# Optimization experiments

Hardware: AMD Instinct MI355X
Metric: run time of the kernel (lower is better)

The kernel has to match this reference:

```python
import jax, jax.numpy as jnp
import numpy as np

B, S, H, KVH, D, MD = 4, 4096, 2, 1, 2, 5  # batch, seq, heads, kv heads, head_dim, model_dim
EPS, SCALE = 1e-6, 16.0


def _rmsnorm(t):
    # RMSNormNoWeight with scale=16.0 over last dim
    var = jnp.mean(t * t, axis=-1, keepdims=True)
    return SCALE * t * jax.lax.rsqrt(var + EPS)


def _rope(t, cos, sin):
    # t: (B, S, h, D); cos/sin: (S, D//2). Complex multiply on interleaved pairs.
    tr, ti = t[..., 0::2], t[..., 1::2]
    c = cos[None, :, None, :]
    s = sin[None, :, None, :]
    out_r = tr * c - ti * s
    out_i = tr * s + ti * c
    return jnp.stack([out_r, out_i], axis=-1).reshape(t.shape)


def setup_inputs() -> dict:
    key = jax.random.key(0)
    ks = jax.random.split(key, 9)
    return {
        "x": jax.random.normal(ks[0], (B, S, MD), jnp.float32),
        "freqs": jax.random.normal(ks[1], (S, D // 2), jnp.float32),
        "shared_qk_v": jax.random.normal(ks[2], (MD,), jnp.float32),
        "shared_v_v": jax.random.normal(ks[3], (MD,), jnp.float32),
        "shared_o_v": jax.random.normal(ks[4], (H * D,), jnp.float32),
        "shared_vproj_u": jax.random.normal(ks[5], (KVH * D,), jnp.float32),
        "q_u": jax.random.normal(ks[6], (H * D,), jnp.float32),
        "k_u": jax.random.normal(ks[7], (KVH * D,), jnp.float32),
        "o_u": jax.random.normal(ks[8], (MD,), jnp.float32),
    }


def reference(x, freqs, shared_qk_v, shared_v_v, shared_o_v, shared_vproj_u, q_u, k_u, o_u):
    b, s = x.shape[0], x.shape[1]
    # rank-1 projections: (x . v) outer u
    s_qk = jnp.sum(x * shared_qk_v, axis=-1, keepdims=True)  # (B,S,1) shared by q and k
    q = (s_qk * q_u).reshape(b, s, H, D)
    k = (s_qk * k_u).reshape(b, s, KVH, D)
    s_v = jnp.sum(x * shared_v_v, axis=-1, keepdims=True)
    v = (s_v * shared_vproj_u).reshape(b, s, KVH, D)
    # qk-norm + rotary
    q = _rmsnorm(q)
    k = _rmsnorm(k)
    cos, sin = jnp.cos(freqs), jnp.sin(freqs)
    q = _rope(q, cos, sin)
    k = _rope(k, cos, sin)
    # (B,h,S,D)
    q = q.transpose(0, 2, 1, 3)
    k = k.transpose(0, 2, 1, 3)
    v = v.transpose(0, 2, 1, 3)
    # GQA repeat kv heads
    k = jnp.repeat(k, H // KVH, axis=1)
    v = jnp.repeat(v, H // KVH, axis=1)
    scores = jnp.einsum('bhqd,bhkd->bhqk', q, k) / jnp.sqrt(jnp.float32(D))
    probs = jax.nn.softmax(scores, axis=-1)
    out = jnp.einsum('bhqk,bhkd->bhqd', probs, v)
    out = out.transpose(0, 2, 1, 3).reshape(b, s, H * D)
    # rank-1 output projection
    s_o = jnp.sum(out * shared_o_v, axis=-1, keepdims=True)
    return s_o * o_u  # (B,S,MODEL_DIM)
```

## Files before the change

kernel.cpp:

```cpp
#include <hip/hip_runtime.h>
#include <math.h>


#define BQ 4
#define SQ 4096
#define MDQ 5
#define EPSQ 1e-6f
#define SCALEQ 16.0f
#define L2E 1.4426950408889634f
#define ISQ2 0.70710678118654752f

typedef float v2f __attribute__((ext_vector_type(2)));

__device__ __forceinline__ float fast_exp2(float x) {
#if __has_builtin(__builtin_amdgcn_exp2f)
    return __builtin_amdgcn_exp2f(x);
#else
    return __expf(x * 0.6931471805599453f);
#endif
}

__global__ __launch_bounds__(256)
void ca_prep(const float* __restrict__ x, const float* __restrict__ freqs,
             const float* __restrict__ qk_v, const float* __restrict__ v_v,
             const float* __restrict__ k_u, float4* __restrict__ pqc)
{
    const int idx = blockIdx.x * 256 + threadIdx.x;
    const int j   = idx & (SQ - 1);

    const float w0 = k_u[0], w1 = k_u[1];
    const float mk = 0.5f * (w0 * w0 + w1 * w1);

    const float qk0 = qk_v[0], qk1 = qk_v[1], qk2 = qk_v[2], qk3 = qk_v[3], qk4 = qk_v[4];
    const float vv0 = v_v[0],  vv1 = v_v[1],  vv2 = v_v[2],  vv3 = v_v[3],  vv4 = v_v[4];

    const float* xr = x + (size_t)idx * MDQ;
    const float x0 = xr[0], x1 = xr[1], x2 = xr[2], x3 = xr[3], x4 = xr[4];
    const float a  = x0*qk0 + x1*qk1 + x2*qk2 + x3*qk3 + x4*qk4;
    const float sv = x0*vv0 + x1*vv1 + x2*vv2 + x3*vv3 + x4*vv4;

    float sj, cj;
    __sincosf(freqs[j], &sj, &cj);
    const float mu = SCALEQ * a * rsqrtf(a * a * mk + EPSQ);
    pqc[idx] = make_float4(mu * cj, mu * sj, sv, sv);
}

#define BLOCK 256
#define RSETS 4
#define RPT 2
#define ROWSB (RSETS * RPT)
#define TILES (SQ / ROWSB)
#define KTILE 256
#define NKT (SQ / KTILE)
#define JPT (KTILE / 64)

__global__ __launch_bounds__(BLOCK)
void ca_main(const float* __restrict__ x,
             const float* __restrict__ freqs,
             const float* __restrict__ qk_v,
             const float* __restrict__ o_v,
             const float* __restrict__ vproj_u,
             const float* __restrict__ q_u,
             const float* __restrict__ k_u,
             const float* __restrict__ o_u,
             const float4* __restrict__ pqc,
             float* __restrict__ out)
{
    __shared__ float4 sKey[2][KTILE];

    const int tid = threadIdx.x;
    const int sp  = tid & 63;
    const int rs  = tid >> 6;
    const int bx  = blockIdx.x;
    const int b   = bx / TILES;
    const int tile = bx % TILES;
    const int i0  = tile * ROWSB + rs * RPT;

    const float w0 = k_u[0], w1 = k_u[1];
    const float mk  = 0.5f * (w0 * w0 + w1 * w1);
    const float Mmu = SCALEQ * rsqrtf(mk);

    const float qk0 = qk_v[0], qk1 = qk_v[1], qk2 = qk_v[2], qk3 = qk_v[3], qk4 = qk_v[4];
    const float u00 = q_u[0], u01 = q_u[1], u10 = q_u[2], u11 = q_u[3];
    const float m0 = 0.5f * (u00 * u00 + u01 * u01);
    const float m1 = 0.5f * (u10 * u10 + u11 * u11);
    const float A0 = u00 * w0 + u01 * w1, B0 = u01 * w0 - u00 * w1;
    const float A1 = u10 * w0 + u11 * w1, B1 = u11 * w0 - u10 * w1;

    v2f al[RPT], be[RPT], Cc[RPT];
#pragma unroll
    for (int k = 0; k < RPT; ++k) {
        const int i = i0 + k;
        const float* xi = x + (size_t)(b * SQ + i) * MDQ;
        const float ai = xi[0]*qk0 + xi[1]*qk1 + xi[2]*qk2 + xi[3]*qk3 + xi[4]*qk4;
        float si, ci;
        __sincosf(freqs[i], &si, &ci);
        const float lam0 = SCALEQ * ai * rsqrtf(ai * ai * m0 + EPSQ);
        const float lam1 = SCALEQ * ai * rsqrtf(ai * ai * m1 + EPSQ);
        const float a0  = lam0 * (A0 * ci - B0 * si) * ISQ2;
        const float b0_ = lam0 * (A0 * si + B0 * ci) * ISQ2;
        const float a1  = lam1 * (A1 * ci - B1 * si) * ISQ2;
        const float b1_ = lam1 * (A1 * si + B1 * ci) * ISQ2;
        const float r0 = sqrtf(a0 * a0 + b0_ * b0_);
        const float r1 = sqrtf(a1 * a1 + b1_ * b1_);
        al[k] = (v2f){a0 * L2E, a1 * L2E};
        be[k] = (v2f){b0_ * L2E, b1_ * L2E};
        Cc[k] = (v2f){-r0 * Mmu * L2E, -r1 * Mmu * L2E};
    }

    const float4* __restrict__ gsrc = pqc + (size_t)b * SQ + tid;

    float4 stage = gsrc[0];
    sKey[0][tid] = stage;
    __syncthreads();

    v2f l[RPT], n[RPT];
#pragma unroll
    for (int k = 0; k < RPT; ++k) { l[k] = (v2f){0.f, 0.f}; n[k] = (v2f){0.f, 0.f}; }

    for (int t = 0; t < NKT; ++t) {
        const int cur = t & 1;
        if (t + 1 < NKT) stage = gsrc[(size_t)(t + 1) * KTILE];

        const float4* kb = &sKey[cur][sp];
#pragma unroll
        for (int jj = 0; jj < JPT; ++jj) {
            const float4 v = kb[jj * 64];
            const v2f vx = (v2f){v.x, v.x};
            const v2f vy = (v2f){v.y, v.y};
            const v2f vz = (v2f){v.z, v.w};
#pragma unroll
            for (int k = 0; k < RPT; ++k) {
                const v2f s = al[k] * vx + (be[k] * vy + Cc[k]);
                v2f e;
                e.x = fast_exp2(s.x);
                e.y = fast_exp2(s.y);
                l[k] += e;
                n[k] += e * vz;
            }
        }

        if (t + 1 < NKT) {
            sKey[cur ^ 1][tid] = stage;
            __syncthreads();
        }
    }

#pragma unroll
    for (int m = 1; m < 64; m <<= 1) {
#pragma unroll
        for (int k = 0; k < RPT; ++k) {
            l[k].x += __shfl_xor(l[k].x, m, 64);
            l[k].y += __shfl_xor(l[k].y, m, 64);
            n[k].x += __shfl_xor(n[k].x, m, 64);
            n[k].y += __shfl_xor(n[k].y, m, 64);
        }
    }

    if (sp < RPT) {
        const int k = sp;
        const float L0 = fmaxf(l[k].x, 1e-30f);
        const float L1 = fmaxf(l[k].y, 1e-30f);
        const float W0 = n[k].x / L0, W1 = n[k].y / L1;

        const float p0 = vproj_u[0], p1 = vproj_u[1];
        const float d0 = p0 * o_v[0] + p1 * o_v[1];
        const float d1 = p0 * o_v[2] + p1 * o_v[3];
        const float so = W0 * d0 + W1 * d1;

        float* orow = out + (size_t)(b * SQ + i0 + k) * MDQ;
        orow[0] = so * o_u[0];
        orow[1] = so * o_u[1];
        orow[2] = so * o_u[2];
        orow[3] = so * o_u[3];
        orow[4] = so * o_u[4];
    }
}

#define FROWS 32
#define FSPLIT 8
#define FJSUB (SQ / FSPLIT)
#define FTILES (SQ / FROWS)

__global__ __launch_bounds__(256)
void ca_fallback(const float* __restrict__ x,
                 const float* __restrict__ freqs,
                 const float* __restrict__ qk_v,
                 const float* __restrict__ v_v,
                 const float* __restrict__ o_v,
                 const float* __restrict__ vproj_u,
                 const float* __restrict__ q_u,
                 const float* __restrict__ k_u,
                 const float* __restrict__ o_u,
                 float* __restrict__ out)
{
    __shared__ float2 sPQ[SQ];
    __shared__ float  sCv[SQ];
    __shared__ float4 sRed[FROWS][FSPLIT];

    const int tid  = threadIdx.x;
    const int b    = blockIdx.x / FTILES;
    const int tile = blockIdx.x % FTILES;

    const float w0 = k_u[0], w1 = k_u[1];
    const float mk  = 0.5f * (w0 * w0 + w1 * w1);
    const float Mmu = SCALEQ * rsqrtf(mk);

    const float qk0 = qk_v[0], qk1 = qk_v[1], qk2 = qk_v[2], qk3 = qk_v[3], qk4 = qk_v[4];
    const float vv0 = v_v[0],  vv1 = v_v[1],  vv2 = v_v[2],  vv3 = v_v[3],  vv4 = v_v[4];

    for (int k = 0; k < SQ / 256; ++k) {
        const int j = tid + k * 256;
        const float* xr = x + (size_t)(b * SQ + j) * MDQ;
        const float x0 = xr[0], x1 = xr[1], x2 = xr[2], x3 = xr[3], x4 = xr[4];
        const float a  = x0*qk0 + x1*qk1 + x2*qk2 + x3*qk3 + x4*qk4;
        const float sv = x0*vv0 + x1*vv1 + x2*vv2 + x3*vv3 + x4*vv4;
        float sj, cj;
        __sincosf(freqs[j], &sj, &cj);
        const float mu = SCALEQ * a * rsqrtf(a * a * mk + EPSQ);
        sPQ[j] = make_float2(mu * cj, mu * sj);
        sCv[j] = sv;
    }

    const int row = tid & (FROWS - 1);
    const int sp  = tid / FROWS;
    const int i   = tile * FROWS + row;

    const float u00 = q_u[0], u01 = q_u[1], u10 = q_u[2], u11 = q_u[3];
    const float m0 = 0.5f * (u00 * u00 + u01 * u01);
    const float m1 = 0.5f * (u10 * u10 + u11 * u11);
    const float A0 = u00 * w0 + u01 * w1, B0 = u01 * w0 - u00 * w1;
    const float A1 = u10 * w0 + u11 * w1, B1 = u11 * w0 - u10 * w1;

    const float* xi = x + (size_t)(b * SQ + i) * MDQ;
    const float ai = xi[0]*qk0 + xi[1]*qk1 + xi[2]*qk2 + xi[3]*qk3 + xi[4]*qk4;
    float si, ci;
    __sincosf(freqs[i], &si, &ci);
    const float lam0 = SCALEQ * ai * rsqrtf(ai * ai * m0 + EPSQ);
    const float lam1 = SCALEQ * ai * rsqrtf(ai * ai * m1 + EPSQ);
    const float alr0 = lam0 * (A0 * ci - B0 * si) * ISQ2;
    const float ber0 = lam0 * (A0 * si + B0 * ci) * ISQ2;
    const float alr1 = lam1 * (A1 * ci - B1 * si) * ISQ2;
    const float ber1 = lam1 * (A1 * si + B1 * ci) * ISQ2;
    const float r0 = sqrtf(alr0 * alr0 + ber0 * ber0);
    const float r1 = sqrtf(alr1 * alr1 + ber1 * ber1);
    const float al0 = alr0 * L2E, be0 = ber0 * L2E, C0 = -r0 * Mmu * L2E;
    const float al1 = alr1 * L2E, be1 = ber1 * L2E, C1 = -r1 * Mmu * L2E;

    __syncthreads();

    const float2* __restrict__ pq  = sPQ + sp * FJSUB;
    const float*  __restrict__ cvp = sCv + sp * FJSUB;
    float l0 = 0.f, n0 = 0.f, l1 = 0.f, n1 = 0.f;
#pragma unroll 8
    for (int jj = 0; jj < FJSUB; ++jj) {
        const float2 v = pq[jj];
        const float cv = cvp[jj];
        const float s0 = fmaf(al0, v.x, fmaf(be0, v.y, C0));
        const float s1 = fmaf(al1, v.x, fmaf(be1, v.y, C1));
        const float e0 = fast_exp2(s0);
        const float e1 = fast_exp2(s1);
        l0 += e0; n0 = fmaf(e0, cv, n0);
        l1 += e1; n1 = fmaf(e1, cv, n1);
    }

    sRed[row][sp] = make_float4(l0, n0, l1, n1);
    __syncthreads();

    if (tid < FROWS) {
        float L0 = 0.f, N0 = 0.f, L1 = 0.f, N1 = 0.f;
#pragma unroll
        for (int s = 0; s < FSPLIT; ++s) {
            const float4 t = sRed[tid][s];
            L0 += t.x; N0 += t.y; L1 += t.z; N1 += t.w;
        }
        L0 = fmaxf(L0, 1e-30f);
        L1 = fmaxf(L1, 1e-30f);
        const float W0 = N0 / L0, W1 = N1 / L1;
        const float p0 = vproj_u[0], p1 = vproj_u[1];
        const float d0 = p0 * o_v[0] + p1 * o_v[1];
        const float d1 = p0 * o_v[2] + p1 * o_v[3];
        const float so = W0 * d0 + W1 * d1;

        const int ig = tile * FROWS + tid;
        float* orow = out + (size_t)(b * SQ + ig) * MDQ;
        orow[0] = so * o_u[0];
        orow[1] = so * o_u[1];
        orow[2] = so * o_u[2];
        orow[3] = so * o_u[3];
        orow[4] = so * o_u[4];
    }
}

extern "C" void kernel_launch(void* const* d_in, const int* in_sizes, int n_in,
                              void* d_out, int out_size, void* d_ws, size_t ws_size,
                              hipStream_t stream) {
    (void)in_sizes; (void)n_in; (void)out_size;
    const float* x       = (const float*)d_in[0];
    const float* freqs   = (const float*)d_in[1];
    const float* qk_v    = (const float*)d_in[2];
    const float* v_v     = (const float*)d_in[3];
    const float* o_v     = (const float*)d_in[4];
    const float* vproj_u = (const float*)d_in[5];
    const float* q_u     = (const float*)d_in[6];
    const float* k_u     = (const float*)d_in[7];
    const float* o_u     = (const float*)d_in[8];
    float* out = (float*)d_out;

    const size_t pqc_bytes = (size_t)BQ * SQ * sizeof(float4);
    if (ws_size >= pqc_bytes) {
        float4* pqc = (float4*)d_ws;
        hipLaunchKernelGGL(ca_prep, dim3(BQ * SQ / 256), dim3(256), 0, stream,
                           x, freqs, qk_v, v_v, k_u, pqc);
        hipLaunchKernelGGL(ca_main, dim3(BQ * TILES), dim3(BLOCK), 0, stream,
                           x, freqs, qk_v, o_v, vproj_u, q_u, k_u, o_u, pqc, out);
    } else {
        hipLaunchKernelGGL(ca_fallback, dim3(BQ * FTILES), dim3(256), 0, stream,
                           x, freqs, qk_v, v_v, o_v, vproj_u, q_u, k_u, o_u, out);
    }
}
```

Measured before the change: 94.46 us.

## Fuse key preprocessing into main attention kernel with full-sequence LDS

Merges the separate key-preparation kernel into the attention kernel. Each 1024-thread block computes all keys for its batch directly into a 64KB shared buffer and then scans them without per-tile double buffering or repeated barriers. This removes a launch, the workspace write and read, and the per-tile synchronisation. In exchange, every block recomputes the key preprocessing, and the large LDS footprint limits how many blocks fit per CU. The workspace fallback path is deleted.

```diff
diff --git a/kernel.cpp b/kernel.cpp
--- a/kernel.cpp
+++ b/kernel.cpp
@@ -20,72 +20,62 @@
 #endif
 }
 
-__global__ __launch_bounds__(256)
-void ca_prep(const float* __restrict__ x, const float* __restrict__ freqs,
-             const float* __restrict__ qk_v, const float* __restrict__ v_v,
-             const float* __restrict__ k_u, float4* __restrict__ pqc)
+#define BLOCK 1024
+#define WAVES 16
+#define RPT 2
+#define ROWSB (WAVES * RPT)
+#define TILES (SQ / ROWSB)
+#define KPT (SQ / BLOCK)
+#define JPT (SQ / 64)
+
+__global__ __launch_bounds__(BLOCK, 8)
+void ca_fused(const float* __restrict__ x,
+              const float* __restrict__ freqs,
+              const float* __restrict__ qk_v,
+              const float* __restrict__ v_v,
+              const float* __restrict__ o_v,
+              const float* __restrict__ vproj_u,
+              const float* __restrict__ q_u,
+              const float* __restrict__ k_u,
+              const float* __restrict__ o_u,
+              float* __restrict__ out)
 {
-    const int idx = blockIdx.x * 256 + threadIdx.x;
-    const int j   = idx & (SQ - 1);
-
-    const float w0 = k_u[0], w1 = k_u[1];
-    const float mk = 0.5f * (w0 * w0 + w1 * w1);
-
-    const float qk0 = qk_v[0], qk1 = qk_v[1], qk2 = qk_v[2], qk3 = qk_v[3], qk4 = qk_v[4];
-    const float vv0 = v_v[0],  vv1 = v_v[1],  vv2 = v_v[2],  vv3 = v_v[3],  vv4 = v_v[4];
-
-    const float* xr = x + (size_t)idx * MDQ;
-    const float x0 = xr[0], x1 = xr[1], x2 = xr[2], x3 = xr[3], x4 = xr[4];
-    const float a  = x0*qk0 + x1*qk1 + x2*qk2 + x3*qk3 + x4*qk4;
-    const float sv = x0*vv0 + x1*vv1 + x2*vv2 + x3*vv3 + x4*vv4;
-
-    float sj, cj;
-    __sincosf(freqs[j], &sj, &cj);
-    const float mu = SCALEQ * a * rsqrtf(a * a * mk + EPSQ);
-    pqc[idx] = make_float4(mu * cj, mu * sj, sv, sv);
-}
-
-#define BLOCK 256
-#define RSETS 4
-#define RPT 2
-#define ROWSB (RSETS * RPT)
-#define TILES (SQ / ROWSB)
-#define KTILE 256
-#define NKT (SQ / KTILE)
-#define JPT (KTILE / 64)
-
-__global__ __launch_bounds__(BLOCK)
-void ca_main(const float* __restrict__ x,
-             const float* __restrict__ freqs,
-             const float* __restrict__ qk_v,
-             const float* __restrict__ o_v,
-             const float* __restrict__ vproj_u,
-             const float* __restrict__ q_u,
-             const float* __restrict__ k_u,
-             const float* __restrict__ o_u,
-             const float4* __restrict__ pqc,
-             float* __restrict__ out)
-{
-    __shared__ float4 sKey[2][KTILE];
+    __shared__ float4 sKey[SQ];
 
     const int tid = threadIdx.x;
     const int sp  = tid & 63;
-    const int rs  = tid >> 6;
+    const int w   = tid >> 6;
     const int bx  = blockIdx.x;
     const int b   = bx / TILES;
     const int tile = bx % TILES;
-    const int i0  = tile * ROWSB + rs * RPT;
 
     const float w0 = k_u[0], w1 = k_u[1];
     const float mk  = 0.5f * (w0 * w0 + w1 * w1);
     const float Mmu = SCALEQ * rsqrtf(mk);
 
     const float qk0 = qk_v[0], qk1 = qk_v[1], qk2 = qk_v[2], qk3 = qk_v[3], qk4 = qk_v[4];
+    const float vv0 = v_v[0],  vv1 = v_v[1],  vv2 = v_v[2],  vv3 = v_v[3],  vv4 = v_v[4];
+
+#pragma unroll
+    for (int kk = 0; kk < KPT; ++kk) {
+        const int j = tid + kk * BLOCK;
+        const float* xr = x + (size_t)(b * SQ + j) * MDQ;
+        const float x0 = xr[0], x1 = xr[1], x2 = xr[2], x3 = xr[3], x4 = xr[4];
+        const float a  = x0*qk0 + x1*qk1 + x2*qk2 + x3*qk3 + x4*qk4;
+        const float sv = x0*vv0 + x1*vv1 + x2*vv2 + x3*vv3 + x4*vv4;
+        float sj, cj;
+        __sincosf(freqs[j], &sj, &cj);
+        const float mu = SCALEQ * a * rsqrtf(a * a * mk + EPSQ);
+        sKey[j] = make_float4(mu * cj, mu * sj, sv, sv);
+    }
+
     const float u00 = q_u[0], u01 = q_u[1], u10 = q_u[2], u11 = q_u[3];
     const float m0 = 0.5f * (u00 * u00 + u01 * u01);
     const float m1 = 0.5f * (u10 * u10 + u11 * u11);
     const float A0 = u00 * w0 + u01 * w1, B0 = u01 * w0 - u00 * w1;
     const float A1 = u10 * w0 + u11 * w1, B1 = u11 * w0 - u10 * w1;
+
+    const int i0 = tile * ROWSB + w * RPT;
 
     v2f al[RPT], be[RPT], Cc[RPT];
 #pragma unroll
@@ -108,41 +98,27 @@
         Cc[k] = (v2f){-r0 * Mmu * L2E, -r1 * Mmu * L2E};
     }
 
-    const float4* __restrict__ gsrc = pqc + (size_t)b * SQ + tid;
-
-    float4 stage = gsrc[0];
-    sKey[0][tid] = stage;
     __syncthreads();
 
     v2f l[RPT], n[RPT];
 #pragma unroll
     for (int k = 0; k < RPT; ++k) { l[k] = (v2f){0.f, 0.f}; n[k] = (v2f){0.f, 0.f}; }
 
-    for (int t = 0; t < NKT; ++t) {
-        const int cur = t & 1;
-        if (t + 1 < NKT) stage = gsrc[(size_t)(t + 1) * KTILE];
-
-        const float4* kb = &sKey[cur][sp];
+    const float4* __restrict__ kb = &sKey[sp];
+#pragma unroll 8
+    for (int jj = 0; jj < JPT; ++jj) {
+        const float4 v = kb[jj * 64];
+        const v2f vx = (v2f){v.x, v.x};
+        const v2f vy = (v2f){v.y, v.y};
+        const v2f vz = (v2f){v.z, v.w};
 #pragma unroll
-        for (int jj = 0; jj < JPT; ++jj) {
-            const float4 v = kb[jj * 64];
-            const v2f vx = (v2f){v.x, v.x};
-            const v2f vy = (v2f){v.y, v.y};
-            const v2f vz = (v2f){v.z, v.w};
-#pragma unroll
-            for (int k = 0; k < RPT; ++k) {
-                const v2f s = al[k] * vx + (be[k] * vy + Cc[k]);
-                v2f e;
-                e.x = fast_exp2(s.x);
-                e.y = fast_exp2(s.y);
-                l[k] += e;
-                n[k] += e * vz;
-            }
-        }
-
-        if (t + 1 < NKT) {
-            sKey[cur ^ 1][tid] = stage;
-            __syncthreads();
+        for (int k = 0; k < RPT; ++k) {
+            const v2f s = al[k] * vx + (be[k] * vy + Cc[k]);
+            v2f e;
+            e.x = fast_exp2(s.x);
+            e.y = fast_exp2(s.y);
+            l[k] += e;
+            n[k] += e * vz;
         }
     }
 
@@ -177,125 +153,10 @@
     }
 }
 
-#define FROWS 32
-#define FSPLIT 8
-#define FJSUB (SQ / FSPLIT)
-#define FTILES (SQ / FROWS)
-
-__global__ __launch_bounds__(256)
-void ca_fallback(const float* __restrict__ x,
-                 const float* __restrict__ freqs,
-                 const float* __restrict__ qk_v,
-                 const float* __restrict__ v_v,
-                 const float* __restrict__ o_v,
-                 const float* __restrict__ vproj_u,
-                 const float* __restrict__ q_u,
-                 const float* __restrict__ k_u,
-                 const float* __restrict__ o_u,
-                 float* __restrict__ out)
-{
-    __shared__ float2 sPQ[SQ];
-    __shared__ float  sCv[SQ];
-    __shared__ float4 sRed[FROWS][FSPLIT];
-
-    const int tid  = threadIdx.x;
-    const int b    = blockIdx.x / FTILES;
-    const int tile = blockIdx.x % FTILES;
-
-    const float w0 = k_u[0], w1 = k_u[1];
-    const float mk  = 0.5f * (w0 * w0 + w1 * w1);
-    const float Mmu = SCALEQ * rsqrtf(mk);
-
-    const float qk0 = qk_v[0], qk1 = qk_v[1], qk2 = qk_v[2], qk3 = qk_v[3], qk4 = qk_v[4];
-    const float vv0 = v_v[0],  vv1 = v_v[1],  vv2 = v_v[2],  vv3 = v_v[3],  vv4 = v_v[4];
-
-    for (int k = 0; k < SQ / 256; ++k) {
-        const int j = tid + k * 256;
-        const float* xr = x + (size_t)(b * SQ + j) * MDQ;
-        const float x0 = xr[0], x1 = xr[1], x2 = xr[2], x3 = xr[3], x4 = xr[4];
-        const float a  = x0*qk0 + x1*qk1 + x2*qk2 + x3*qk3 + x4*qk4;
-        const float sv = x0*vv0 + x1*vv1 + x2*vv2 + x3*vv3 + x4*vv4;
-        float sj, cj;
-        __sincosf(freqs[j], &sj, &cj);
-        const float mu = SCALEQ * a * rsqrtf(a * a * mk + EPSQ);
-        sPQ[j] = make_float2(mu * cj, mu * sj);
-        sCv[j] = sv;
-    }
-
-    const int row = tid & (FROWS - 1);
-    const int sp  = tid / FROWS;
-    const int i   = tile * FROWS + row;
-
-    const float u00 = q_u[0], u01 = q_u[1], u10 = q_u[2], u11 = q_u[3];
-    const float m0 = 0.5f * (u00 * u00 + u01 * u01);
-    const float m1 = 0.5f * (u10 * u10 + u11 * u11);
-    const float A0 = u00 * w0 + u01 * w1, B0 = u01 * w0 - u00 * w1;
-    const float A1 = u10 * w0 + u11 * w1, B1 = u11 * w0 - u10 * w1;
-
-    const float* xi = x + (size_t)(b * SQ + i) * MDQ;
-    const float ai = xi[0]*qk0 + xi[1]*qk1 + xi[2]*qk2 + xi[3]*qk3 + xi[4]*qk4;
-    float si, ci;
-    __sincosf(freqs[i], &si, &ci);
-    const float lam0 = SCALEQ * ai * rsqrtf(ai * ai * m0 + EPSQ);
-    const float lam1 = SCALEQ * ai * rsqrtf(ai * ai * m1 + EPSQ);
-    const float alr0 = lam0 * (A0 * ci - B0 * si) * ISQ2;
-    const float ber0 = lam0 * (A0 * si + B0 * ci) * ISQ2;
-    const float alr1 = lam1 * (A1 * ci - B1 * si) * ISQ2;
-    const float ber1 = lam1 * (A1 * si + B1 * ci) * ISQ2;
-    const float r0 = sqrtf(alr0 * alr0 + ber0 * ber0);
-    const float r1 = sqrtf(alr1 * alr1 + ber1 * ber1);
-    const float al0 = alr0 * L2E, be0 = ber0 * L2E, C0 = -r0 * Mmu * L2E;
-    const float al1 = alr1 * L2E, be1 = ber1 * L2E, C1 = -r1 * Mmu * L2E;
-
-    __syncthreads();
-
-    const float2* __restrict__ pq  = sPQ + sp * FJSUB;
-    const float*  __restrict__ cvp = sCv + sp * FJSUB;
-    float l0 = 0.f, n0 = 0.f, l1 = 0.f, n1 = 0.f;
-#pragma unroll 8
-    for (int jj = 0; jj < FJSUB; ++jj) {
-        const float2 v = pq[jj];
-        const float cv = cvp[jj];
-        const float s0 = fmaf(al0, v.x, fmaf(be0, v.y, C0));
-        const float s1 = fmaf(al1, v.x, fmaf(be1, v.y, C1));
-        const float e0 = fast_exp2(s0);
-        const float e1 = fast_exp2(s1);
-        l0 += e0; n0 = fmaf(e0, cv, n0);
-        l1 += e1; n1 = fmaf(e1, cv, n1);
-    }
-
-    sRed[row][sp] = make_float4(l0, n0, l1, n1);
-    __syncthreads();
-
-    if (tid < FROWS) {
-        float L0 = 0.f, N0 = 0.f, L1 = 0.f, N1 = 0.f;
-#pragma unroll
-        for (int s = 0; s < FSPLIT; ++s) {
-            const float4 t = sRed[tid][s];
-            L0 += t.x; N0 += t.y; L1 += t.z; N1 += t.w;
-        }
-        L0 = fmaxf(L0, 1e-30f);
-        L1 = fmaxf(L1, 1e-30f);
-        const float W0 = N0 / L0, W1 = N1 / L1;
-        const float p0 = vproj_u[0], p1 = vproj_u[1];
-        const float d0 = p0 * o_v[0] + p1 * o_v[1];
-        const float d1 = p0 * o_v[2] + p1 * o_v[3];
-        const float so = W0 * d0 + W1 * d1;
-
-        const int ig = tile * FROWS + tid;
-        float* orow = out + (size_t)(b * SQ + ig) * MDQ;
-        orow[0] = so * o_u[0];
-        orow[1] = so * o_u[1];
-        orow[2] = so * o_u[2];
-        orow[3] = so * o_u[3];
-        orow[4] = so * o_u[4];
-    }
-}
-
 extern "C" void kernel_launch(void* const* d_in, const int* in_sizes, int n_in,
                               void* d_out, int out_size, void* d_ws, size_t ws_size,
                               hipStream_t stream) {
-    (void)in_sizes; (void)n_in; (void)out_size;
+    (void)in_sizes; (void)n_in; (void)out_size; (void)d_ws; (void)ws_size;
     const float* x       = (const float*)d_in[0];
     const float* freqs   = (const float*)d_in[1];
     const float* qk_v    = (const float*)d_in[2];
@@ -307,15 +168,6 @@
     const float* o_u     = (const float*)d_in[8];
     float* out = (float*)d_out;
 
-    const size_t pqc_bytes = (size_t)BQ * SQ * sizeof(float4);
-    if (ws_size >= pqc_bytes) {
-        float4* pqc = (float4*)d_ws;
-        hipLaunchKernelGGL(ca_prep, dim3(BQ * SQ / 256), dim3(256), 0, stream,
-                           x, freqs, qk_v, v_v, k_u, pqc);
-        hipLaunchKernelGGL(ca_main, dim3(BQ * TILES), dim3(BLOCK), 0, stream,
-                           x, freqs, qk_v, o_v, vproj_u, q_u, k_u, o_u, pqc, out);
-    } else {
-        hipLaunchKernelGGL(ca_fallback, dim3(BQ * FTILES), dim3(256), 0, stream,
-                           x, freqs, qk_v, v_v, o_v, vproj_u, q_u, k_u, o_u, out);
-    }
+    hipLaunchKernelGGL(ca_fused, dim3(BQ * TILES), dim3(BLOCK), 0, stream,
+                       x, freqs, qk_v, v_v, o_v, vproj_u, q_u, k_u, o_u, out);
 }
```

Measured after the change: 94.68 us. No clear change (+0.2%).
